# Optimization experiments

Measured on AMD Instinct MI355X. Metric: run time of the kernel, lower is better.

## Reference

```python
import jax, jax.numpy as jnp
import numpy as np

EPS = 1e-5

def _layernorm(x, g, b):
    m = jnp.mean(x, axis=-1, keepdims=True)
    v = jnp.var(x, axis=-1, keepdims=True)
    return (x - m) * jax.lax.rsqrt(v + EPS) * g + b

def setup_inputs() -> dict:
    key = jax.random.key(0)
    ks = jax.random.split(key, 8)
    B, N, D, H = 4, 2048, 1024, 16
    F = 2 * D
    s = 0.02
    return {
        "x": jax.random.normal(ks[0], (B, N, D), jnp.float32),
        "mask": jnp.zeros((B, N, N), jnp.float32),
        "Wq": jax.random.normal(ks[1], (D, D), jnp.float32) * s,
        "Wk": jax.random.normal(ks[2], (D, D), jnp.float32) * s,
        "Wv": jax.random.normal(ks[3], (D, D), jnp.float32) * s,
        "Wc": jax.random.normal(ks[4], (D, D), jnp.float32) * s,
        "bc": jnp.zeros((D,), jnp.float32),
        "W1": jax.random.normal(ks[5], (D, F), jnp.float32) * s,
        "b1": jnp.zeros((F,), jnp.float32),
        "W2": jax.random.normal(ks[6], (F, D), jnp.float32) * s,
        "b2": jnp.zeros((D,), jnp.float32),
        "g1": jnp.ones((D,), jnp.float32),
        "be1": jnp.zeros((D,), jnp.float32),
        "g2": jnp.ones((D,), jnp.float32),
        "be2": jnp.zeros((D,), jnp.float32),
    }

def reference(x, mask, Wq, Wk, Wv, Wc, bc, W1, b1, W2, b2, g1, be1, g2, be2):
    B, N, D = x.shape
    H = 16
    Dh = D // H
    scale = 1.0 / np.sqrt(Dh).astype(np.float32)
    # projections -> [B, H, N, Dh]
    def heads(t):
        return t.reshape(B, N, H, Dh).transpose(0, 2, 1, 3)
    q = heads(x @ Wq)
    k = heads(x @ Wk)
    v = heads(x @ Wv)
    score = jnp.einsum('bhnd,bhmd->bhnm', q, k) * scale + mask[:, None, :, :]
    attn = jnp.einsum('bhnm,bhmd->bhnd', jax.nn.softmax(score, axis=-1), v)
    attn = attn.transpose(0, 2, 1, 3).reshape(B, N, D)
    x = x + attn @ Wc + bc
    x = _layernorm(x, g1, be1)
    x = x + jnp.maximum(x @ W1 + b1, 0.0) @ W2 + b2
    x = _layernorm(x, g2, be2)
    return x
```

## Files before the change

kernel.cpp:

```cpp
#include <hip/hip_runtime.h>
#include <hip/hip_bf16.h>


#define DEV __device__ __forceinline__

using s16x8 = __attribute__((ext_vector_type(8))) short;
using f32x4 = __attribute__((ext_vector_type(4))) float;

DEV unsigned short f2bf(float f) {
  unsigned u = __float_as_uint(f);
  u += 0x7fffu + ((u >> 16) & 1u);
  return (unsigned short)(u >> 16);
}
DEV unsigned pack2bf(float a, float b) {
  return (unsigned)f2bf(a) | ((unsigned)f2bf(b) << 16);
}
DEV unsigned cvt_pk_bf16(float lo, float hi) {
  unsigned r;
  asm("v_cvt_pk_bf16_f32 %0, %1, %2" : "=v"(r) : "v"(lo), "v"(hi));
  return r;
}

typedef __attribute__((address_space(3))) unsigned lds_u32_t;
typedef const __attribute__((address_space(1))) unsigned glb_u32_t;

DEV void gld_lds16(const void* g, void* l) {
  __builtin_amdgcn_global_load_lds((glb_u32_t*)g, (lds_u32_t*)l, 16, 0, 0);
}

template<int RELU, int RESID, int OUTF>
__global__ __launch_bounds__(256)
void gemm_bt(const unsigned short* __restrict__ A, const unsigned short* __restrict__ Bt,
             unsigned short* __restrict__ Cb, float* __restrict__ Cf,
             const float* __restrict__ bias, const float* __restrict__ resid,
             int M, int N, int K)
{
  __shared__ unsigned short As[128 * 32];
  __shared__ unsigned short Bs[128 * 32];
  const int tid  = threadIdx.x;
  const int wave = tid >> 6, lane = tid & 63;
  const int g = lane >> 4, q = lane & 15;

  const int nwg  = gridDim.x * gridDim.y;
  const int flat = blockIdx.y * gridDim.x + blockIdx.x;
  const int rm   = (nwg & 7) ? flat : ((flat & 7) * (nwg >> 3) + (flat >> 3));
  const int m0 = (rm / gridDim.x) * 128, n0 = (rm % gridDim.x) * 128;
  const int wr = wave >> 1, wc = wave & 1;

  f32x4 acc[4][4] = {};

  const int i0 = wave * 512 + lane * 8;
  const int i1 = 2048 + i0;

  for (int kt = 0; kt < K; kt += 32) {
    gld_lds16(A  + (size_t)(m0 + (i0 >> 5)) * K + kt + (i0 & 31), As + wave * 512);
    gld_lds16(Bt + (size_t)(n0 + (i0 >> 5)) * K + kt + (i0 & 31), Bs + wave * 512);
    gld_lds16(A  + (size_t)(m0 + (i1 >> 5)) * K + kt + (i1 & 31), As + 2048 + wave * 512);
    gld_lds16(Bt + (size_t)(n0 + (i1 >> 5)) * K + kt + (i1 & 31), Bs + 2048 + wave * 512);
    __syncthreads();
    s16x8 a[4], b[4];
#pragma unroll
    for (int m = 0; m < 4; ++m)
      a[m] = *(const s16x8*)(As + (wr * 64 + m * 16 + q) * 32 + g * 8);
#pragma unroll
    for (int n = 0; n < 4; ++n)
      b[n] = *(const s16x8*)(Bs + (wc * 64 + n * 16 + q) * 32 + g * 8);
#pragma unroll
    for (int m = 0; m < 4; ++m)
#pragma unroll
      for (int n = 0; n < 4; ++n)
        acc[m][n] = __builtin_amdgcn_mfma_f32_16x16x32_bf16(a[m], b[n], acc[m][n], 0, 0, 0);
    __syncthreads();
  }

#pragma unroll
  for (int n = 0; n < 4; ++n) {
    const int col = n0 + wc * 64 + n * 16 + q;
    const float bv = bias ? bias[col] : 0.0f;
#pragma unroll
    for (int m = 0; m < 4; ++m) {
      const int row0 = m0 + wr * 64 + m * 16 + g * 4;
#pragma unroll
      for (int r = 0; r < 4; ++r) {
        float v = acc[m][n][r] + bv;
        if (RELU) v = fmaxf(v, 0.0f);
        if (RESID) v += resid[(size_t)(row0 + r) * N + col];
        if (OUTF) Cf[(size_t)(row0 + r) * N + col] = v;
        else      Cb[(size_t)(row0 + r) * N + col] = f2bf(v);
      }
    }
  }
}

__global__ __launch_bounds__(256, 4)
void attn_kernel(const unsigned short* __restrict__ qkv,
                 const unsigned short* __restrict__ vt,
                 const float* __restrict__ mask,
                 unsigned short* __restrict__ outb)
{
  __shared__ unsigned short Ks[2][4096];
  __shared__ unsigned short Vs[2][4096];
  __shared__ unsigned short Pl[4][1024];
  const int tid = threadIdx.x, wave = tid >> 6, lane = tid & 63;
  const int g = lane >> 4, q = lane & 15;

  const int flat = blockIdx.y * 32 + blockIdx.x;
  const int rm   = (flat & 7) * 256 + (flat >> 3);
  const int qt = rm & 31, bh = rm >> 5;
  const int b = bh >> 4, h = bh & 15;
  const int qrow = qt * 64 + wave * 16;
  const size_t tok0 = (size_t)b * 2048;

  const unsigned short* Qp = qkv + (tok0 + qrow + q) * 3072 + h * 64;
  const s16x8 bq0 = *(const s16x8*)(Qp + g * 8);
  const s16x8 bq1 = *(const s16x8*)(Qp + 32 + g * 8);
  const float* Mp = mask + ((size_t)b * 2048 + qrow + q) * 2048;

  const int lr = lane >> 3;
  const int sc = (lane & 7) ^ lr;
  const unsigned short* Kg = qkv + tok0 * 3072 + 1024 + h * 64
                           + (size_t)(wave * 16 + lr) * 3072 + sc * 8;
  const unsigned short* Vg = vt + ((size_t)bh * 64 + wave * 16 + lr) * 2048 + sc * 8;
  unsigned short* KsW = Ks[0] + wave * 1024;
  unsigned short* VsW = Vs[0] + wave * 1024;

  auto STAGE = [&](int buf, int t) {
    const size_t ko = (size_t)t * (64 * 3072);
    const int    vo = t * 64;
    gld_lds16(Kg + ko,            KsW + buf * 4096);
    gld_lds16(Kg + ko + 8 * 3072, KsW + buf * 4096 + 512);
    gld_lds16(Vg + vo,            VsW + buf * 4096);
    gld_lds16(Vg + vo + 8 * 2048, VsW + buf * 4096 + 512);
  };

  f32x4 ot[4] = {};
  f32x4 mkc[4], mkn[4];
  float mrun = -3.0e38f, lsum = 0.0f;
  char* Pw = (char*)&Pl[wave][0];

  STAGE(0, 0);
#pragma unroll
  for (int m2 = 0; m2 < 4; ++m2) mkc[m2] = *(const f32x4*)(Mp + m2 * 16 + g * 4);
  __syncthreads();

  int cur = 0;
  for (int t = 0; t < 32; ++t) {
    if (t < 31) {
      STAGE(cur ^ 1, t + 1);
#pragma unroll
      for (int m2 = 0; m2 < 4; ++m2)
        mkn[m2] = *(const f32x4*)(Mp + (t + 1) * 64 + m2 * 16 + g * 4);
    }
    const unsigned short* Kt = Ks[cur];
    const unsigned short* Vt = Vs[cur];

    f32x4 st[4] = {};
    __builtin_amdgcn_s_setprio(1);
#pragma unroll
    for (int m2 = 0; m2 < 4; ++m2) {
      const unsigned short* kp = Kt + (m2 * 16 + q) * 64;
      const s16x8 ak0 = *(const s16x8*)(kp + ((g       ^ (q & 7)) * 8));
      const s16x8 ak1 = *(const s16x8*)(kp + (((g + 4) ^ (q & 7)) * 8));
      st[m2] = __builtin_amdgcn_mfma_f32_16x16x32_bf16(ak0, bq0, st[m2], 0, 0, 0);
      st[m2] = __builtin_amdgcn_mfma_f32_16x16x32_bf16(ak1, bq1, st[m2], 0, 0, 0);
    }
    __builtin_amdgcn_s_setprio(0);

    float tmax = -3.0e38f;
#pragma unroll
    for (int m2 = 0; m2 < 4; ++m2) {
#pragma unroll
      for (int r = 0; r < 4; ++r) {
        st[m2][r] = st[m2][r] * 0.125f + mkc[m2][r];
        tmax = fmaxf(tmax, st[m2][r]);
      }
    }
    tmax = fmaxf(tmax, __shfl_xor(tmax, 16));
    tmax = fmaxf(tmax, __shfl_xor(tmax, 32));
    const float mnew  = fmaxf(mrun, tmax);
    const float alpha = __expf(mrun - mnew);
    mrun = mnew;

    float rsum = 0.0f;
#pragma unroll
    for (int m2 = 0; m2 < 4; ++m2) {
#pragma unroll
      for (int r = 0; r < 4; ++r) {
        st[m2][r] = __expf(st[m2][r] - mnew);
        rsum += st[m2][r];
      }
      const int bir  = m2 * 32 + g * 8;
      const int addr = q * 128 + ((((bir >> 4) ^ (q & 7))) << 4) + (bir & 15);
      uint2 pk;
      pk.x = cvt_pk_bf16(st[m2][0], st[m2][1]);
      pk.y = cvt_pk_bf16(st[m2][2], st[m2][3]);
      *(uint2*)(Pw + addr) = pk;
    }
    rsum += __shfl_xor(rsum, 16);
    rsum += __shfl_xor(rsum, 32);
    lsum = lsum * alpha + rsum;
#pragma unroll
    for (int m = 0; m < 4; ++m) {
      ot[m][0] *= alpha; ot[m][1] *= alpha; ot[m][2] *= alpha; ot[m][3] *= alpha;
    }

    __builtin_amdgcn_s_setprio(1);
#pragma unroll
    for (int kb = 0; kb < 2; ++kb) {
      const int blk = (kb * 4 + g) ^ (q & 7);
      const s16x8 pb = *(const s16x8*)(Pw + q * 128 + blk * 16);
#pragma unroll
      for (int m = 0; m < 4; ++m) {
        const s16x8 av = *(const s16x8*)(Vt + (m * 16 + q) * 64 + blk * 8);
        ot[m] = __builtin_amdgcn_mfma_f32_16x16x32_bf16(av, pb, ot[m], 0, 0, 0);
      }
    }
    __builtin_amdgcn_s_setprio(0);

#pragma unroll
    for (int m2 = 0; m2 < 4; ++m2) mkc[m2] = mkn[m2];
    __syncthreads();
    cur ^= 1;
  }

  const float inv = 1.0f / lsum;
#pragma unroll
  for (int m = 0; m < 4; ++m) {
    const int bir  = m * 32 + g * 8;
    const int addr = q * 128 + (((bir >> 4) ^ (q & 7)) << 4) + (bir & 15);
    uint2 pk;
    pk.x = cvt_pk_bf16(ot[m][0] * inv, ot[m][1] * inv);
    pk.y = cvt_pk_bf16(ot[m][2] * inv, ot[m][3] * inv);
    *(uint2*)(Pw + addr) = pk;
  }
#pragma unroll
  for (int p = 0; p < 2; ++p) {
    const int c  = p * 64 + lane;
    const int qq = c >> 3, cc = c & 7;
    const int blk = cc ^ (qq & 7);
    const s16x8 vv = *(const s16x8*)(Pw + qq * 128 + blk * 16);
    *(s16x8*)(outb + (tok0 + qrow + qq) * 1024 + h * 64 + cc * 8) = vv;
  }
}

__global__ __launch_bounds__(256)
void ln_kernel(const float* __restrict__ in, float* __restrict__ outf,
               unsigned short* __restrict__ outb,
               const float* __restrict__ gam, const float* __restrict__ bet)
{
  __shared__ float red[8];
  const int row = blockIdx.x, tid = threadIdx.x;
  const f32x4 v = *(const f32x4*)(in + (size_t)row * 1024 + tid * 4);
  float s  = v[0] + v[1] + v[2] + v[3];
  float ss = v[0]*v[0] + v[1]*v[1] + v[2]*v[2] + v[3]*v[3];
#pragma unroll
  for (int o = 1; o < 64; o <<= 1) { s += __shfl_xor(s, o); ss += __shfl_xor(ss, o); }
  if ((tid & 63) == 0) { red[tid >> 6] = s; red[4 + (tid >> 6)] = ss; }
  __syncthreads();
  s  = red[0] + red[1] + red[2] + red[3];
  ss = red[4] + red[5] + red[6] + red[7];
  const float mean = s * (1.0f / 1024.0f);
  const float var  = ss * (1.0f / 1024.0f) - mean * mean;
  const float rstd = rsqrtf(var + 1e-5f);
  const f32x4 gm = *(const f32x4*)(gam + tid * 4);
  const f32x4 bt = *(const f32x4*)(bet + tid * 4);
  f32x4 o;
#pragma unroll
  for (int j = 0; j < 4; ++j) o[j] = (v[j] - mean) * rstd * gm[j] + bt[j];
  if (outf) *(f32x4*)(outf + (size_t)row * 1024 + tid * 4) = o;
  if (outb) {
    uint2 pk; pk.x = pack2bf(o[0], o[1]); pk.y = pack2bf(o[2], o[3]);
    *(uint2*)(outb + (size_t)row * 1024 + tid * 4) = pk;
  }
}

__global__ __launch_bounds__(256)
void tcast_kernel(const float* __restrict__ in, unsigned short* __restrict__ out, int R, int C)
{
  __shared__ float t[32][33];
  const int tx = threadIdx.x & 31, ty = threadIdx.x >> 5;
  const int c0 = blockIdx.x * 32, r0 = blockIdx.y * 32;
#pragma unroll
  for (int k = 0; k < 4; ++k)
    t[ty + k * 8][tx] = in[(size_t)(r0 + ty + k * 8) * C + c0 + tx];
  __syncthreads();
#pragma unroll
  for (int k = 0; k < 4; ++k)
    out[(size_t)(c0 + ty + k * 8) * R + r0 + tx] = f2bf(t[tx][ty + k * 8]);
}

__global__ __launch_bounds__(256)
void tv_kernel(const unsigned short* __restrict__ qkv, unsigned short* __restrict__ vt)
{
  __shared__ unsigned short t[32][33];
  const int tx = threadIdx.x & 31, ty = threadIdx.x >> 5;
  const int c0 = blockIdx.x * 32, r0 = blockIdx.y * 32, b = blockIdx.z;
  const unsigned short* in = qkv + (size_t)b * 2048 * 3072 + 2048;
  unsigned short* out = vt + (size_t)b * 1024 * 2048;
#pragma unroll
  for (int k = 0; k < 4; ++k)
    t[ty + k * 8][tx] = in[(size_t)(r0 + ty + k * 8) * 3072 + c0 + tx];
  __syncthreads();
#pragma unroll
  for (int k = 0; k < 4; ++k)
    out[(size_t)(c0 + ty + k * 8) * 2048 + r0 + tx] = t[tx][ty + k * 8];
}

__global__ __launch_bounds__(256)
void cast_x_kernel(const float* __restrict__ in, unsigned short* __restrict__ out)
{
  const size_t i = ((size_t)blockIdx.x * 256 + threadIdx.x) * 4;
  const f32x4 v = *(const f32x4*)(in + i);
  uint2 pk; pk.x = pack2bf(v[0], v[1]); pk.y = pack2bf(v[2], v[3]);
  *(uint2*)(out + i) = pk;
}

extern "C" void kernel_launch(void* const* d_in, const int* in_sizes, int n_in,
                              void* d_out, int out_size, void* d_ws, size_t ws_size,
                              hipStream_t stream)
{
  (void)in_sizes; (void)n_in; (void)out_size; (void)ws_size;
  const float* x   = (const float*)d_in[0];
  const float* msk = (const float*)d_in[1];
  const float* Wq  = (const float*)d_in[2];
  const float* Wk  = (const float*)d_in[3];
  const float* Wv  = (const float*)d_in[4];
  const float* Wc  = (const float*)d_in[5];
  const float* bc  = (const float*)d_in[6];
  const float* W1  = (const float*)d_in[7];
  const float* b1  = (const float*)d_in[8];
  const float* W2  = (const float*)d_in[9];
  const float* b2  = (const float*)d_in[10];
  const float* g1  = (const float*)d_in[11];
  const float* be1 = (const float*)d_in[12];
  const float* g2  = (const float*)d_in[13];
  const float* be2 = (const float*)d_in[14];
  float* out = (float*)d_out;
  char* ws = (char*)d_ws;
  const size_t MB = 1u << 20;
  unsigned short* xb    = (unsigned short*)(ws + 0 * MB);
  unsigned short* wqkvt = (unsigned short*)(ws + 16 * MB);
  unsigned short* wct   = (unsigned short*)(ws + 22 * MB);
  unsigned short* w1t   = (unsigned short*)(ws + 24 * MB);
  unsigned short* w2t   = (unsigned short*)(ws + 28 * MB);
  unsigned short* qkv   = (unsigned short*)(ws + 32 * MB);
  unsigned short* vt    = (unsigned short*)(ws + 80 * MB);
  unsigned short* attnb = xb;
  float*          y1    = (float*)(ws + 32 * MB);
  unsigned short* h1b   = (unsigned short*)(ws + 64 * MB);
  float*          h1f   = (float*)(ws + 96 * MB);
  unsigned short* midb  = (unsigned short*)(ws + 128 * MB);

  cast_x_kernel<<<8192, 256, 0, stream>>>(x, xb);
  tcast_kernel<<<dim3(32, 32), 256, 0, stream>>>(Wq, wqkvt,               1024, 1024);
  tcast_kernel<<<dim3(32, 32), 256, 0, stream>>>(Wk, wqkvt + 1024 * 1024, 1024, 1024);
  tcast_kernel<<<dim3(32, 32), 256, 0, stream>>>(Wv, wqkvt + 2048 * 1024, 1024, 1024);
  tcast_kernel<<<dim3(32, 32), 256, 0, stream>>>(Wc, wct,                 1024, 1024);
  tcast_kernel<<<dim3(64, 32), 256, 0, stream>>>(W1, w1t,                 1024, 2048);
  tcast_kernel<<<dim3(32, 64), 256, 0, stream>>>(W2, w2t,                 2048, 1024);

  gemm_bt<0, 0, 0><<<dim3(24, 64), 256, 0, stream>>>(xb, wqkvt, qkv, nullptr,
                                                     nullptr, nullptr, 8192, 3072, 1024);
  tv_kernel<<<dim3(32, 64, 4), 256, 0, stream>>>(qkv, vt);
  attn_kernel<<<dim3(32, 64), 256, 0, stream>>>(qkv, vt, msk, attnb);
  gemm_bt<0, 1, 1><<<dim3(8, 64), 256, 0, stream>>>(attnb, wct, nullptr, y1,
                                                    bc, x, 8192, 1024, 1024);
  ln_kernel<<<8192, 256, 0, stream>>>(y1, h1f, h1b, g1, be1);
  gemm_bt<1, 0, 0><<<dim3(16, 64), 256, 0, stream>>>(h1b, w1t, midb, nullptr,
                                                     b1, nullptr, 8192, 2048, 1024);
  gemm_bt<0, 1, 1><<<dim3(8, 64), 256, 0, stream>>>(midb, w2t, nullptr, out,
                                                    b2, h1f, 8192, 1024, 2048);
  ln_kernel<<<8192, 256, 0, stream>>>(out, out, nullptr, g2, be2);
}
```

Before: 470.6 us.

## Add 256x256 eight-wave GEMM with fused V transpose and lazy softmax rescale

Adds a new 512-thread GEMM kernel with 256x256 tiles, 64-wide K steps and double-buffered direct-to-LDS loads. It is used for the QKV projection and the FFN up-projection. For QKV it writes the V part directly in transposed layout, so the separate transpose kernel is removed. The attention softmax now works in exp2 form and skips the running-max rescale unless the max grows by more than a threshold. The larger tiles and lazy rescale trade register and LDS pressure and a small risk of exp overflow for more data reuse and fewer launches and ALU ops. The transposed V stores are strided writes, which may be uncoalesced.

```diff
diff --git a/kernel.cpp b/kernel.cpp
--- a/kernel.cpp
+++ b/kernel.cpp
@@ -20,12 +20,138 @@
   asm("v_cvt_pk_bf16_f32 %0, %1, %2" : "=v"(r) : "v"(lo), "v"(hi));
   return r;
 }
+DEV f32x4 vmax4(f32x4 a, f32x4 b) {
+  f32x4 r;
+  r[0] = fmaxf(a[0], b[0]); r[1] = fmaxf(a[1], b[1]);
+  r[2] = fmaxf(a[2], b[2]); r[3] = fmaxf(a[3], b[3]);
+  return r;
+}
 
 typedef __attribute__((address_space(3))) unsigned lds_u32_t;
 typedef const __attribute__((address_space(1))) unsigned glb_u32_t;
 
 DEV void gld_lds16(const void* g, void* l) {
   __builtin_amdgcn_global_load_lds((glb_u32_t*)g, (lds_u32_t*)l, 16, 0, 0);
+}
+
+template<int RELU, int VOUT>
+__global__ __launch_bounds__(512, 2)
+void gemm8p(const unsigned short* __restrict__ A, const unsigned short* __restrict__ Bt,
+            unsigned short* __restrict__ Cb, const float* __restrict__ bias,
+            unsigned short* __restrict__ vtout, int M, int N, int K)
+{
+  __shared__ unsigned short Sh[2][2][256 * 64];
+  const int tid = threadIdx.x;
+  const int w = tid >> 6, lane = tid & 63;
+  const int g = lane >> 4, q = lane & 15;
+  const int wr = w >> 2, wc = w & 3;
+
+  const int nwg  = gridDim.x * gridDim.y;
+  const int flat = blockIdx.y * gridDim.x + blockIdx.x;
+  const int rm   = (flat & 7) * (nwg >> 3) + (flat >> 3);
+  const int m0 = (rm / gridDim.x) * 256, n0 = (rm % gridDim.x) * 256;
+
+  f32x4 acc[8][4] = {};
+
+  const int srow = w * 8 + (lane >> 3);
+  const int scol = ((lane & 7) ^ (lane >> 3)) * 8;
+  const unsigned short* Ag = A  + (size_t)(m0 + srow) * K + scol;
+  const unsigned short* Bg = Bt + (size_t)(n0 + srow) * K + scol;
+
+  auto STG = [&](const unsigned short* Gb, int buf, int ab, int half, int kt) {
+    const unsigned short* gs = Gb + (size_t)(half * 128) * K + kt * 64;
+    unsigned short* ls = &Sh[buf][ab][(half * 128 + w * 8) * 64];
+    gld_lds16(gs, ls);
+    gld_lds16(gs + (size_t)64 * K, ls + 64 * 64);
+  };
+  auto LDA = [&](int buf, int mq, s16x8 af[4][2]) {
+#pragma unroll
+    for (int mm = 0; mm < 4; ++mm) {
+      const unsigned short* rp = &Sh[buf][0][(wr * 128 + mq * 64 + mm * 16 + q) * 64];
+#pragma unroll
+      for (int kk = 0; kk < 2; ++kk)
+        af[mm][kk] = *(const s16x8*)(rp + (((kk * 4 + g) ^ (q & 7)) * 8));
+    }
+  };
+  auto LDB = [&](int buf, int nq, s16x8 bf[2][2]) {
+#pragma unroll
+    for (int nn = 0; nn < 2; ++nn) {
+      const unsigned short* rp = &Sh[buf][1][(wc * 64 + nq * 32 + nn * 16 + q) * 64];
+#pragma unroll
+      for (int kk = 0; kk < 2; ++kk)
+        bf[nn][kk] = *(const s16x8*)(rp + (((kk * 4 + g) ^ (q & 7)) * 8));
+    }
+  };
+  auto MQ = [&](int mq, int nq, const s16x8 af[4][2], const s16x8 bf[2][2]) {
+    __builtin_amdgcn_s_setprio(1);
+#pragma unroll
+    for (int kk = 0; kk < 2; ++kk)
+#pragma unroll
+      for (int mm = 0; mm < 4; ++mm)
+#pragma unroll
+        for (int nn = 0; nn < 2; ++nn)
+          acc[mq * 4 + mm][nq * 2 + nn] = __builtin_amdgcn_mfma_f32_16x16x32_bf16(
+              af[mm][kk], bf[nn][kk], acc[mq * 4 + mm][nq * 2 + nn], 0, 0, 0);
+    __builtin_amdgcn_s_setprio(0);
+  };
+  auto BAR = [&]() { __builtin_amdgcn_sched_barrier(0); __builtin_amdgcn_s_barrier(); };
+
+  STG(Ag, 0, 0, 0, 0); STG(Ag, 0, 0, 1, 0);
+  STG(Bg, 0, 1, 0, 0); STG(Bg, 0, 1, 1, 0);
+
+  const int NKT = K >> 6;
+  s16x8 af[4][2], bf0[2][2], bf1[2][2];
+#pragma unroll 1
+  for (int kt = 0; kt < NKT; ++kt) {
+    const int b = kt & 1, sb = b ^ 1, kn = kt + 1;
+    const bool stg = (kn < NKT);
+    if (stg) { STG(Ag, sb, 0, 0, kn); asm volatile("s_waitcnt vmcnt(2)" ::: "memory"); }
+    else     {                        asm volatile("s_waitcnt vmcnt(0)" ::: "memory"); }
+    BAR();
+    LDA(b, 0, af); LDB(b, 0, bf0);
+    MQ(0, 0, af, bf0);
+    BAR();
+    if (stg) STG(Ag, sb, 0, 1, kn);
+    LDB(b, 1, bf1);
+    MQ(0, 1, af, bf1);
+    BAR();
+    if (stg) STG(Bg, sb, 1, 0, kn);
+    LDA(b, 1, af);
+    MQ(1, 0, af, bf0);
+    BAR();
+    if (stg) STG(Bg, sb, 1, 1, kn);
+    MQ(1, 1, af, bf1);
+    BAR();
+  }
+
+#pragma unroll
+  for (int n = 0; n < 4; ++n) {
+    const int col = n0 + wc * 64 + n * 16 + q;
+    if (VOUT && col >= 2048) {
+      const int cv = col - 2048;
+#pragma unroll
+      for (int m = 0; m < 8; ++m) {
+        const int row0 = m0 + wr * 128 + m * 16 + g * 4;
+        const int bb = row0 >> 11;
+        ushort4 pk;
+        pk.x = f2bf(acc[m][n][0]); pk.y = f2bf(acc[m][n][1]);
+        pk.z = f2bf(acc[m][n][2]); pk.w = f2bf(acc[m][n][3]);
+        *(ushort4*)(vtout + ((size_t)bb * 1024 + cv) * 2048 + (row0 & 2047)) = pk;
+      }
+    } else {
+      const float bv = bias ? bias[col] : 0.0f;
+#pragma unroll
+      for (int m = 0; m < 8; ++m) {
+        const int row0 = m0 + wr * 128 + m * 16 + g * 4;
+#pragma unroll
+        for (int r = 0; r < 4; ++r) {
+          float v = acc[m][n][r] + bv;
+          if (RELU) v = fmaxf(v, 0.0f);
+          Cb[(size_t)(row0 + r) * N + col] = f2bf(v);
+        }
+      }
+    }
+  }
 }
 
 template<int RELU, int RESID, int OUTF>
@@ -135,8 +261,10 @@
 
   f32x4 ot[4] = {};
   f32x4 mkc[4], mkn[4];
-  float mrun = -3.0e38f, lsum = 0.0f;
+  float mrun = -3.0e38f, mnl = 0.0f, lsum = 0.0f;
   char* Pw = (char*)&Pl[wave][0];
+  const float SC  = 0.125f;
+  const float L2E = 1.4426950408889634f;
 
   STAGE(0, 0);
 #pragma unroll
@@ -144,6 +272,7 @@
   __syncthreads();
 
   int cur = 0;
+#pragma unroll 1
   for (int t = 0; t < 32; ++t) {
     if (t < 31) {
       STAGE(cur ^ 1, t + 1);
@@ -166,31 +295,37 @@
     }
     __builtin_amdgcn_s_setprio(0);
 
-    float tmax = -3.0e38f;
-#pragma unroll
-    for (int m2 = 0; m2 < 4; ++m2) {
-#pragma unroll
-      for (int r = 0; r < 4; ++r) {
-        st[m2][r] = st[m2][r] * 0.125f + mkc[m2][r];
-        tmax = fmaxf(tmax, st[m2][r]);
-      }
-    }
+#pragma unroll
+    for (int m2 = 0; m2 < 4; ++m2)
+#pragma unroll
+      for (int r = 0; r < 4; ++r)
+        st[m2][r] = fmaf(st[m2][r], SC, mkc[m2][r]);
+
+    f32x4 a0 = vmax4(vmax4(st[0], st[1]), vmax4(st[2], st[3]));
+    float tmax = fmaxf(fmaxf(a0[0], a0[1]), fmaxf(a0[2], a0[3]));
     tmax = fmaxf(tmax, __shfl_xor(tmax, 16));
     tmax = fmaxf(tmax, __shfl_xor(tmax, 32));
-    const float mnew  = fmaxf(mrun, tmax);
-    const float alpha = __expf(mrun - mnew);
-    mrun = mnew;
+
+    if (!__all(tmax <= mrun + 8.0f)) {
+      const float mn = fmaxf(mrun, tmax);
+      const float al = exp2f((mrun - mn) * L2E);
+      mrun = mn; mnl = mn * L2E;
+      lsum *= al;
+#pragma unroll
+      for (int m = 0; m < 4; ++m) {
+        ot[m][0] *= al; ot[m][1] *= al; ot[m][2] *= al; ot[m][3] *= al;
+      }
+    }
 
     float rsum = 0.0f;
 #pragma unroll
     for (int m2 = 0; m2 < 4; ++m2) {
 #pragma unroll
-      for (int r = 0; r < 4; ++r) {
-        st[m2][r] = __expf(st[m2][r] - mnew);
-        rsum += st[m2][r];
-      }
+      for (int r = 0; r < 4; ++r)
+        st[m2][r] = exp2f(fmaf(st[m2][r], L2E, -mnl));
+      rsum += (st[m2][0] + st[m2][1]) + (st[m2][2] + st[m2][3]);
       const int bir  = m2 * 32 + g * 8;
-      const int addr = q * 128 + ((((bir >> 4) ^ (q & 7))) << 4) + (bir & 15);
+      const int addr = q * 128 + (((bir >> 4) ^ (q & 7)) << 4) + (bir & 15);
       uint2 pk;
       pk.x = cvt_pk_bf16(st[m2][0], st[m2][1]);
       pk.y = cvt_pk_bf16(st[m2][2], st[m2][3]);
@@ -198,11 +333,7 @@
     }
     rsum += __shfl_xor(rsum, 16);
     rsum += __shfl_xor(rsum, 32);
-    lsum = lsum * alpha + rsum;
-#pragma unroll
-    for (int m = 0; m < 4; ++m) {
-      ot[m][0] *= alpha; ot[m][1] *= alpha; ot[m][2] *= alpha; ot[m][3] *= alpha;
-    }
+    lsum += rsum;
 
     __builtin_amdgcn_s_setprio(1);
 #pragma unroll
@@ -287,23 +418,6 @@
 #pragma unroll
   for (int k = 0; k < 4; ++k)
     out[(size_t)(c0 + ty + k * 8) * R + r0 + tx] = f2bf(t[tx][ty + k * 8]);
-}
-
-__global__ __launch_bounds__(256)
-void tv_kernel(const unsigned short* __restrict__ qkv, unsigned short* __restrict__ vt)
-{
-  __shared__ unsigned short t[32][33];
-  const int tx = threadIdx.x & 31, ty = threadIdx.x >> 5;
-  const int c0 = blockIdx.x * 32, r0 = blockIdx.y * 32, b = blockIdx.z;
-  const unsigned short* in = qkv + (size_t)b * 2048 * 3072 + 2048;
-  unsigned short* out = vt + (size_t)b * 1024 * 2048;
-#pragma unroll
-  for (int k = 0; k < 4; ++k)
-    t[ty + k * 8][tx] = in[(size_t)(r0 + ty + k * 8) * 3072 + c0 + tx];
-  __syncthreads();
-#pragma unroll
-  for (int k = 0; k < 4; ++k)
-    out[(size_t)(c0 + ty + k * 8) * 2048 + r0 + tx] = t[tx][ty + k * 8];
 }
 
 __global__ __launch_bounds__(256)
@@ -359,15 +473,14 @@
   tcast_kernel<<<dim3(64, 32), 256, 0, stream>>>(W1, w1t,                 1024, 2048);
   tcast_kernel<<<dim3(32, 64), 256, 0, stream>>>(W2, w2t,                 2048, 1024);
 
-  gemm_bt<0, 0, 0><<<dim3(24, 64), 256, 0, stream>>>(xb, wqkvt, qkv, nullptr,
-                                                     nullptr, nullptr, 8192, 3072, 1024);
-  tv_kernel<<<dim3(32, 64, 4), 256, 0, stream>>>(qkv, vt);
+  gemm8p<0, 1><<<dim3(12, 32), 512, 0, stream>>>(xb, wqkvt, qkv, nullptr, vt,
+                                                 8192, 3072, 1024);
   attn_kernel<<<dim3(32, 64), 256, 0, stream>>>(qkv, vt, msk, attnb);
   gemm_bt<0, 1, 1><<<dim3(8, 64), 256, 0, stream>>>(attnb, wct, nullptr, y1,
                                                     bc, x, 8192, 1024, 1024);
   ln_kernel<<<8192, 256, 0, stream>>>(y1, h1f, h1b, g1, be1);
-  gemm_bt<1, 0, 0><<<dim3(16, 64), 256, 0, stream>>>(h1b, w1t, midb, nullptr,
-                                                     b1, nullptr, 8192, 2048, 1024);
+  gemm8p<1, 0><<<dim3(8, 32), 512, 0, stream>>>(h1b, w1t, midb, b1, nullptr,
+                                                8192, 2048, 1024);
   gemm_bt<0, 1, 1><<<dim3(8, 64), 256, 0, stream>>>(midb, w2t, nullptr, out,
                                                     b2, h1f, 8192, 1024, 2048);
   ln_kernel<<<8192, 256, 0, stream>>>(out, out, nullptr, g2, be2);
```

Result: faster. 453.7 us (-3.6%).
